# Optimization experiments

Measured on AMD Instinct MI355X. Metric: run time of the kernel, lower is better.

The kernel has to match this reference:

```python
import jax, jax.numpy as jnp
import numpy as np

EPS = 1e-5

def conv2d(x, w, b, groups=1):
    out = jax.lax.conv_general_dilated(
        x, w, (1, 1), 'SAME',
        dimension_numbers=('NCHW', 'OIHW', 'NCHW'),
        feature_group_count=groups)
    return out + b[None, :, None, None]

def bilinear_gather(img, ys, xs):
    # img [B,C,H,W]; ys,xs [B,K,H,W] float sample coords; zero padding outside
    H, W = img.shape[2], img.shape[3]
    y0 = jnp.floor(ys)
    x0 = jnp.floor(xs)
    wy = ys - y0
    wx = xs - x0

    def corner(yi, xi, w):
        valid = (yi >= 0) & (yi <= H - 1) & (xi >= 0) & (xi <= W - 1)
        yc = jnp.clip(yi, 0, H - 1).astype(jnp.int32)
        xc = jnp.clip(xi, 0, W - 1).astype(jnp.int32)
        # gather -> [B,C,K,H,W]
        v = jax.vmap(lambda im, y, x: im[:, y, x])(img, yc, xc)
        return v * (w * valid)[:, None]

    return (corner(y0, x0, (1 - wy) * (1 - wx))
            + corner(y0, x0 + 1, (1 - wy) * wx)
            + corner(y0 + 1, x0, wy * (1 - wx))
            + corner(y0 + 1, x0 + 1, wy * wx))

def deform_conv(x, offset, w, b):
    # torchvision DeformConv2d, kernel 3x3, stride 1, pad 1; offset layout [B,2*K,H,W] as (dy,dx) per tap
    B, C, H, W = x.shape
    K = 9
    ky = (jnp.repeat(jnp.arange(3), 3) - 1).astype(x.dtype)  # [9]
    kx = (jnp.tile(jnp.arange(3), 3) - 1).astype(x.dtype)
    off = offset.reshape(B, K, 2, H, W)
    base_y = jnp.arange(H, dtype=x.dtype)[None, None, :, None]
    base_x = jnp.arange(W, dtype=x.dtype)[None, None, None, :]
    ys = base_y + ky[None, :, None, None] + off[:, :, 0]  # [B,K,H,W]
    xs = base_x + kx[None, :, None, None] + off[:, :, 1]
    sampled = bilinear_gather(x, ys, xs)                  # [B,C,K,H,W]
    out = jnp.einsum('bckhw,ock->bohw', sampled, w.reshape(w.shape[0], C, K))
    return out + b[None, :, None, None]

def setup_inputs() -> dict:
    key = jax.random.key(0)
    ks = jax.random.split(key, 12)
    C, O = 128, 128
    B, H, W = 4, 96, 96
    s = 0.05
    return {
        'x': jax.random.normal(ks[0], (B, C, H, W), jnp.float32),
        'dw_w': jax.random.normal(ks[1], (C, 1, 3, 3), jnp.float32) * s,
        'dw_b': jax.random.normal(ks[2], (C,), jnp.float32) * s,
        'pw_w': jax.random.normal(ks[3], (O, C, 1, 1), jnp.float32) * s,
        'pw_b': jax.random.normal(ks[4], (O,), jnp.float32) * s,
        'off_w': jax.random.normal(ks[5], (18, O, 3, 3), jnp.float32) * s,
        'off_b': jax.random.normal(ks[6], (18,), jnp.float32) * s,
        'dc_w': jax.random.normal(ks[7], (O, O, 3, 3), jnp.float32) * s,
        'dc_b': jax.random.normal(ks[8], (O,), jnp.float32) * s,
        'ln_g': jnp.ones((O,), jnp.float32),
        'ln_b': jnp.zeros((O,), jnp.float32),
    }

def reference(x, dw_w, dw_b, pw_w, pw_b, off_w, off_b, dc_w, dc_b, ln_g, ln_b):
    C = x.shape[1]
    # depthwise-separable conv
    h = conv2d(x, dw_w, dw_b, groups=C)
    h = conv2d(h, pw_w, pw_b)
    # InstanceNorm2d (affine=False)
    mu = h.mean((2, 3), keepdims=True)
    var = h.var((2, 3), keepdims=True)
    dsc = (h - mu) * jax.lax.rsqrt(var + EPS)
    # Dropout2d: inference mode -> identity
    offset = conv2d(dsc, off_w, off_b)              # [B,18,H,W]
    dc = deform_conv(dsc, offset, dc_w, dc_b)       # [B,O,H,W]
    # LayerNorm over channels (NHWC last axis)
    nhwc = dc.transpose(0, 2, 3, 1)
    m = nhwc.mean(-1, keepdims=True)
    v = nhwc.var(-1, keepdims=True)
    ln = (nhwc - m) * jax.lax.rsqrt(v + EPS) * ln_g + ln_b
    attn = jax.nn.sigmoid(ln.transpose(0, 3, 1, 2))
    return dsc * attn
```

## Files before the change

kernel.cpp:

```cpp
#include <hip/hip_runtime.h>
#include <math.h>

#define HW 9216
#define WD 96
#define NC 128

typedef unsigned short u16;
typedef __attribute__((ext_vector_type(8))) short short8;
typedef __attribute__((ext_vector_type(4))) float v4f;

__device__ __forceinline__ int rfl(int v){ return __builtin_amdgcn_readfirstlane(v); }
__device__ __forceinline__ float bu2f(u16 s){ return __uint_as_float(((unsigned)s)<<16); }
__device__ __forceinline__ u16 f2b(float f){ unsigned u = __float_as_uint(f);
  return (u16)((u + 0x7fffu + ((u>>16)&1u))>>16); }

__global__ __launch_bounds__(256) void prep_weights(const float* __restrict__ pw_w,
    const float* __restrict__ off_w, const float* __restrict__ dc_w,
    u16* __restrict__ wpwb, u16* __restrict__ wob, u16* __restrict__ wdcb){
  int t = blockIdx.x*256 + threadIdx.x;
  if (t < 16384) wpwb[t] = f2b(pw_w[t]);
  if (t < 36864){
    int ntl = t/18432, rem = t - ntl*18432;
    int s = rem>>9, l = (rem>>3)&63, e = rem&7;
    int o = ntl*16 + (l&15);
    int c = (s&3)*32 + ((l>>4)<<3) + e;
    int k = s>>2;
    wob[t] = (o<18) ? f2b(off_w[(o*128+c)*9+k]) : (u16)0;
  }
  if (t < 147456){
    int e = t&7, l = (t>>3)&63, f = (t>>9)&7, g = t>>12;
    int s = g%18, r = g/18;
    int nt = f>>1, ks = f&1;
    int c = ((s&1)<<6) + ks*32 + ((l>>4)<<3) + e;
    int o = (r<<6) + nt*16 + (l&15);
    int k = s>>1;
    wdcb[t] = f2b(dc_w[(o*128+c)*9 + k]);
  }
}

__global__ __launch_bounds__(256) void dw_conv(const float* __restrict__ x,
    const float* __restrict__ w, const float* __restrict__ bias, u16* __restrict__ h1b){
  int n = blockIdx.x*256 + threadIdx.x;
  int bc = rfl(n / 2304);
  int qp = n - bc*2304;
  int p = qp*4;
  int c = bc & 127;
  int yy = p / WD, xx = p - yy*WD;
  const float* xc = x + (size_t)bc*HW;
  const float* wc = w + c*9;
  float bs = bias[c];
  float a0=bs, a1=bs, a2=bs, a3=bs;
  #pragma unroll
  for (int r=0;r<3;r++){
    int y2 = yy + r - 1;
    if (y2>=0 && y2<96){
      const float* row = xc + y2*WD + xx;
      float4 vc = *(const float4*)row;
      float vl = (xx>0)  ? row[-1] : 0.f;
      float vr = (xx<92) ? row[4]  : 0.f;
      float w0 = wc[r*3+0], w1 = wc[r*3+1], w2 = wc[r*3+2];
      a0 = fmaf(w0, vl,   fmaf(w1, vc.x, fmaf(w2, vc.y, a0)));
      a1 = fmaf(w0, vc.x, fmaf(w1, vc.y, fmaf(w2, vc.z, a1)));
      a2 = fmaf(w0, vc.y, fmaf(w1, vc.z, fmaf(w2, vc.w, a2)));
      a3 = fmaf(w0, vc.z, fmaf(w1, vc.w, fmaf(w2, vr,   a3)));
    }
  }
  ushort4 pk = make_ushort4(f2b(a0), f2b(a1), f2b(a2), f2b(a3));
  *(ushort4*)(h1b + (size_t)bc*HW + p) = pk;
}

__global__ __launch_bounds__(256) void pw_mfma(const u16* __restrict__ h1b,
    const u16* __restrict__ wpwb, const float* __restrict__ pw_b,
    u16* __restrict__ h2b){
  __shared__ short Aw[128*136];
  __shared__ short Bw[128*68];
  int blk = blockIdx.x; int row0 = blk*64;
  int b = rfl(row0/HW); int pbase = rfl(row0 - b*HW);
  int t = threadIdx.x;
  #pragma unroll
  for (int i=0;i<8;i++){
    int idx = i*256 + t; int o = idx>>4, seg = idx&15;
    *(short8*)&Aw[o*136 + seg*8] = *(const short8*)(wpwb + o*128 + seg*8);
  }
  #pragma unroll
  for (int i=0;i<4;i++){
    int idx = i*256 + t; int c = idx>>3, seg = idx&7;
    *(short8*)&Bw[c*68 + seg*8] =
      *(const short8*)(h1b + (size_t)(b*NC+c)*HW + pbase + seg*8);
  }
  __syncthreads();
  int w = rfl(t>>6); int l = t&63; int q = l>>4; int ln = l&15;
  v4f acc[8];
  #pragma unroll
  for (int mt=0;mt<8;mt++) acc[mt] = (v4f){0.f,0.f,0.f,0.f};
  #pragma unroll
  for (int ks=0;ks<4;ks++){
    short8 bf;
    #pragma unroll
    for (int j=0;j<8;j++) bf[j] = Bw[(ks*32 + q*8 + j)*68 + w*16 + ln];
    #pragma unroll
    for (int mt=0;mt<8;mt++){
      short8 af = *(short8*)&Aw[(mt*16+ln)*136 + ks*32 + q*8];
      acc[mt] = __builtin_amdgcn_mfma_f32_16x16x32_bf16(af, bf, acc[mt], 0,0,0);
    }
  }
  int px = pbase + w*16 + ln;
  #pragma unroll
  for (int mt=0;mt<8;mt++){
    #pragma unroll
    for (int r=0;r<4;r++){
      int o = mt*16 + q*4 + r;
      h2b[(size_t)(b*NC+o)*HW + px] = f2b(acc[mt][r] + pw_b[o]);
    }
  }
}

__global__ __launch_bounds__(256) void inorm_stats(const u16* __restrict__ h2b,
    float* __restrict__ st){
  int bc = blockIdx.x;
  const u16* src = h2b + (size_t)bc*HW;
  float s=0.f, ss=0.f;
  for (int i=threadIdx.x; i<1152; i+=256){
    short8 v8 = *(const short8*)(src + i*8);
    #pragma unroll
    for (int j=0;j<8;j++){
      float v = bu2f((u16)v8[j]);
      s += v; ss = fmaf(v,v,ss);
    }
  }
  #pragma unroll
  for (int off=32; off; off>>=1){ s += __shfl_down(s,off); ss += __shfl_down(ss,off); }
  __shared__ float rsm[2][4];
  int wave = threadIdx.x>>6, lane = threadIdx.x&63;
  if (lane==0){ rsm[0][wave]=s; rsm[1][wave]=ss; }
  __syncthreads();
  if (threadIdx.x==0){
    float S = rsm[0][0]+rsm[0][1]+rsm[0][2]+rsm[0][3];
    float SS= rsm[1][0]+rsm[1][1]+rsm[1][2]+rsm[1][3];
    float mu = S * (1.f/9216.f);
    float var = SS * (1.f/9216.f) - mu*mu;
    st[bc*2]   = mu;
    st[bc*2+1] = rsqrtf(var + 1e-5f);
  }
}

__global__ __launch_bounds__(256) void make_dsc(const u16* __restrict__ h2b,
    const float* __restrict__ st, u16* __restrict__ dscT){
  int blk = blockIdx.x;
  int pt = blk % 144; int r = blk/144; int ch = r & 1; int b = r >> 1;
  int c0 = ch*64, pbase = pt*64;
  __shared__ float tile[64][65];
  int tr = threadIdx.x >> 2;
  int g  = threadIdx.x & 3;
  int c  = c0 + tr;
  float mu = st[(b*128+c)*2];
  float rs = st[(b*128+c)*2+1];
  const u16* src = h2b + (size_t)(b*128+c)*HW + pbase + g*16;
  #pragma unroll
  for (int i=0;i<2;i++){
    short8 v8 = *(const short8*)(src + i*8);
    #pragma unroll
    for (int j=0;j<8;j++){
      float v = (bu2f((u16)v8[j]) - mu)*rs;
      tile[tr][g*16 + i*8 + j] = v;
    }
  }
  __syncthreads();
  int pr = tr;
  u16* dt = dscT + ((size_t)b*HW + pbase + pr)*NC + c0 + g*16;
  #pragma unroll
  for (int i=0;i<4;i++){
    float v0 = tile[g*16+i*4+0][pr], v1 = tile[g*16+i*4+1][pr];
    float v2 = tile[g*16+i*4+2][pr], v3 = tile[g*16+i*4+3][pr];
    ushort4 hi = make_ushort4(f2b(v0), f2b(v1), f2b(v2), f2b(v3));
    *(ushort4*)(dt + i*4) = hi;
  }
}

__global__ __launch_bounds__(256) void off_mfma(const u16* __restrict__ dscT,
    const u16* __restrict__ wobp, const float* __restrict__ off_b,
    float4* __restrict__ wg, ushort4* __restrict__ ad){
  __shared__ short As[2][32*40];
  __shared__ float Po[18*32];
  int blk = blockIdx.x;
  int tile = (blk&7)*144 + (blk>>3);
  int row0 = tile*32;
  int b = rfl(row0/HW); int pbase = rfl(row0 - b*HW);
  int t = threadIdx.x;
  bool stg = t < 128;
  int apx = (t>>2)&31, segA = t&3;
  int w = rfl(t>>6); int l = t&63; int q = l>>4; int ln = l&15;
  int mt = w&1, ntl = w>>1;
  int P = pbase + apx;
  int py = P/96, px_ = P - 96*py;
  const u16* gsrc = dscT + (size_t)b*HW*NC;
  const u16* wbase = wobp + ntl*18432 + l*8;
  uint4 rgA, rgB; short8 bregE, bregO;
  auto issue = [&](int s, uint4& rg){
    int k = s>>2, cseg = s&3;
    int y2 = py + k/3 - 1, x2 = px_ + k%3 - 1;
    bool valid = stg && ((unsigned)y2 < 96u) && ((unsigned)x2 < 96u);
    int off = ((y2*96 + x2)*NC) + cseg*32 + segA*8;
    rg = valid ? *(const uint4*)(gsrc + off) : (uint4){0,0,0,0};
  };
  auto issueB = [&](int s)->short8{
    return *(const short8*)(wbase + s*512);
  };
  auto commit = [&](int buf, uint4& rg){
    if (stg) *(short8*)&As[buf][apx*40 + segA*8] = *(short8*)&rg;
  };
  v4f acc = (v4f){0.f,0.f,0.f,0.f};
  auto step = [&](int buf, short8 bf){
    short8 ah = *(short8*)&As[buf][(mt*16+ln)*40 + q*8];
    acc = __builtin_amdgcn_mfma_f32_16x16x32_bf16(ah, bf, acc, 0,0,0);
  };
  issue(0, rgA); issue(1, rgB);
  bregE = issueB(0); bregO = issueB(1);
  commit(0, rgA);
  __syncthreads();
  #pragma unroll 1
  for (int s=0;s<36;s+=2){
    if (s+2<36) issue(s+2, rgA);
    commit(1, rgB);
    step(0, bregE);
    if (s+2<36) bregE = issueB(s+2);
    __syncthreads();
    if (s+3<36) issue(s+3, rgB);
    if (s+2<36) commit(0, rgA);
    step(1, bregO);
    if (s+3<36) bregO = issueB(s+3);
    __syncthreads();
  }
  int o = ntl*16 + ln;
  if (o < 18){
    float ob = off_b[o];
    #pragma unroll
    for (int r=0;r<4;r++) Po[o*32 + mt*16 + q*4 + r] = acc[r] + ob;
  }
  __syncthreads();
  #pragma unroll
  for (int i=0;i<2;i++){
    int idx = i*256 + t;
    if (idx < 288){
      int pxl = idx & 31, k = idx >> 5;
      int Pp = pbase + pxl;
      float dy = Po[(2*k)*32 + pxl], dx = Po[(2*k+1)*32 + pxl];
      float ys = (float)(Pp/96 + k/3 - 1) + dy;
      float xs = (float)(Pp%96 + k%3 - 1) + dx;
      float fy0 = floorf(ys), fx0 = floorf(xs);
      float wy = ys - fy0, wx = xs - fx0;
      int y0 = (int)fy0, x0 = (int)fx0;
      int y1 = y0+1, x1 = x0+1;
      float vy0 = (y0>=0 && y0<=95) ? 1.f : 0.f;
      float vy1 = (y1>=0 && y1<=95) ? 1.f : 0.f;
      float vx0 = (x0>=0 && x0<=95) ? 1.f : 0.f;
      float vx1 = (x1>=0 && x1<=95) ? 1.f : 0.f;
      int y0c=min(max(y0,0),95), y1c=min(max(y1,0),95);
      int x0c=min(max(x0,0),95), x1c=min(max(x1,0),95);
      float4 w4;
      w4.x = (1.f-wy)*(1.f-wx)*vy0*vx0;
      w4.y = (1.f-wy)*wx*vy0*vx1;
      w4.z = wy*(1.f-wx)*vy1*vx0;
      w4.w = wy*wx*vy1*vx1;
      int gi = (b*9 + k)*HW + pbase + pxl;
      wg[gi] = w4;
      ad[gi] = make_ushort4((u16)(y0c*WD+x0c), (u16)(y0c*WD+x1c),
                            (u16)(y1c*WD+x0c), (u16)(y1c*WD+x1c));
    }
  }
}

__global__ __launch_bounds__(256) void deform_mfma(const u16* __restrict__ dscT,
    const u16* __restrict__ wdcb, const float* __restrict__ dc_b,
    const float4* __restrict__ wg, const ushort4* __restrict__ ad,
    const float* __restrict__ ln_g, const float* __restrict__ ln_b,
    float* __restrict__ out){
  __shared__ short As[2][32*68];
  __shared__ float4 WgL[288];
  __shared__ ushort4 AdL[288];
  __shared__ float RS[2][4][4][4];
  __shared__ u16 DT[32*128];
  int blk = blockIdx.x;
  int tile = (blk&7)*144 + (blk>>3);
  int row0 = tile*32;
  int b = rfl(row0/HW); int pbase = rfl(row0 - b*HW);
  int t = threadIdx.x;
  int apx = t>>3, cs8 = t&7;
  int w = rfl(t>>6); int l = t&63; int q = l>>4; int ln = l&15;
  int mt = w&1, nb = (w>>1)*4, rrole = rfl(w>>1);
  const u16* db0 = dscT + (size_t)b*HW*NC + cs8*8;
  const u16* wbase = wdcb + (size_t)rrole*(18*4096) + l*8;
  #pragma unroll
  for (int i=0;i<2;i++){
    int idx = i*256 + t;
    if (idx < 288){ int k = idx>>5, pxl = idx&31; int gi = (b*9+k)*HW + pbase + pxl;
      WgL[idx] = wg[gi]; AdL[idx] = ad[gi]; }
  }
  __syncthreads();
  uint4 gA0,gA1,gA2,gA3, gB0,gB1,gB2,gB3;
  float4 wvA, wvB;
  short8 bregE[8], bregO[8];
  auto issueG = [&](int s, float4& wv, uint4& r0, uint4& r1, uint4& r2, uint4& r3){
    int k = s>>1, cb = (s&1)<<6;
    ushort4 av = AdL[k*32+apx]; wv = WgL[k*32+apx];
    const u16* db = db0 + cb;
    r0 = *(const uint4*)(db + (int)av.x*NC);
    r1 = *(const uint4*)(db + (int)av.y*NC);
    r2 = *(const uint4*)(db + (int)av.z*NC);
    r3 = *(const uint4*)(db + (int)av.w*NC);
  };
  auto issueB = [&](int s, short8* dst){
    const u16* p = wbase + s*4096;
    #pragma unroll
    for (int f=0;f<8;f++) dst[f] = *(const short8*)(p + f*512);
  };
  auto commitA = [&](int buf, float4 wv, uint4& r0, uint4& r1, uint4& r2, uint4& r3){
    const u16* pa=(const u16*)&r0; const u16* pb=(const u16*)&r1;
    const u16* pc=(const u16*)&r2; const u16* pd=(const u16*)&r3;
    short8 sv;
    #pragma unroll
    for (int j=0;j<8;j++){
      float f = wv.x*bu2f(pa[j]) + wv.y*bu2f(pb[j]) + wv.z*bu2f(pc[j]) + wv.w*bu2f(pd[j]);
      sv[j] = (short)f2b(f);
    }
    *(short8*)&As[buf][apx*68 + cs8*8] = sv;
  };
  v4f acc[4];
  #pragma unroll
  for (int nt=0;nt<4;nt++) acc[nt] = (v4f){0.f,0.f,0.f,0.f};
  auto step = [&](int buf, const short8* bb){
    #pragma unroll
    for (int ks=0;ks<2;ks++){
      short8 af = *(const short8*)&As[buf][(mt*16+ln)*68 + ks*32 + q*8];
      #pragma unroll
      for (int nt=0;nt<4;nt++)
        acc[nt] = __builtin_amdgcn_mfma_f32_16x16x32_bf16(af, bb[nt*2+ks], acc[nt], 0,0,0);
    }
  };
  issueG(0, wvA, gA0,gA1,gA2,gA3); issueB(0, bregE);
  issueG(1, wvB, gB0,gB1,gB2,gB3); issueB(1, bregO);
  commitA(0, wvA, gA0,gA1,gA2,gA3);
  __syncthreads();
  #pragma unroll 1
  for (int s=0;s<18;s+=2){
    if (s+2<18) issueG(s+2, wvA, gA0,gA1,gA2,gA3);
    commitA(1, wvB, gB0,gB1,gB2,gB3);
    step(0, bregE);
    if (s+2<18) issueB(s+2, bregE);
    __syncthreads();
    if (s+3<18) issueG(s+3, wvB, gB0,gB1,gB2,gB3);
    if (s+2<18) commitA(0, wvA, gA0,gA1,gA2,gA3);
    step(1, bregO);
    if (s+3<18) issueB(s+3, bregO);
    __syncthreads();
  }
  int o_[4]; float bias_[4], g_[4], bb_[4];
  #pragma unroll
  for (int nt=0;nt<4;nt++){
    int o = (nb+nt)*16 + ln;
    o_[nt] = o; bias_[nt] = dc_b[o]; g_[nt] = ln_g[o]; bb_[nt] = ln_b[o];
  }
  float s_[4] = {0.f,0.f,0.f,0.f}, ss_[4] = {0.f,0.f,0.f,0.f};
  #pragma unroll
  for (int r=0;r<4;r++){
    #pragma unroll
    for (int nt=0;nt<4;nt++){
      float v = acc[nt][r] + bias_[nt];
      s_[r] += v; ss_[r] = fmaf(v, v, ss_[r]);
    }
  }
  #pragma unroll
  for (int off=1; off<16; off<<=1){
    #pragma unroll
    for (int r=0;r<4;r++){
      s_[r]  += __shfl_xor(s_[r],  off);
      ss_[r] += __shfl_xor(ss_[r], off);
    }
  }
  if (ln==0){
    #pragma unroll
    for (int r=0;r<4;r++){ RS[0][w][q][r] = s_[r]; RS[1][w][q][r] = ss_[r]; }
  }
  {
    const u16* dsrc = dscT + ((size_t)b*HW + pbase)*NC;
    #pragma unroll
    for (int i=0;i<2;i++){
      int idx = i*256 + t;
      *(short8*)&DT[idx*8] = *(const short8*)(dsrc + idx*8);
    }
  }
  __syncthreads();
  float m_[4], rs_[4];
  #pragma unroll
  for (int r=0;r<4;r++){
    float S  = RS[0][w][q][r] + RS[0][w^2][q][r];
    float SS = RS[1][w][q][r] + RS[1][w^2][q][r];
    float m = S*(1.f/128.f);
    float var = SS*(1.f/128.f) - m*m;
    m_[r] = m; rs_[r] = rsqrtf(var + 1e-5f);
  }
  int pxb = pbase + mt*16 + q*4;
  int lpx = mt*16 + q*4;
  #pragma unroll
  for (int nt=0;nt<4;nt++){
    size_t base = (size_t)(b*NC + o_[nt])*HW + pxb;
    float4 ov;
    #pragma unroll
    for (int r=0;r<4;r++){
      float v = acc[nt][r] + bias_[nt];
      float lnv = (v - m_[r])*rs_[r]*g_[nt] + bb_[nt];
      float attn = 1.f/(1.f+__expf(-lnv));
      float dv = bu2f(DT[(lpx+r)*128 + o_[nt]]);
      ((float*)&ov)[r] = dv * attn;
    }
    *(float4*)(out + base) = ov;
  }
}

extern "C" void kernel_launch(void* const* d_in, const int* in_sizes, int n_in,
                              void* d_out, int out_size, void* d_ws, size_t ws_size,
                              hipStream_t stream){
  const float* x    = (const float*)d_in[0];
  const float* dw_w = (const float*)d_in[1];
  const float* dw_b = (const float*)d_in[2];
  const float* pw_w = (const float*)d_in[3];
  const float* pw_b = (const float*)d_in[4];
  const float* off_w= (const float*)d_in[5];
  const float* off_b= (const float*)d_in[6];
  const float* dc_w = (const float*)d_in[7];
  const float* dc_b = (const float*)d_in[8];
  const float* ln_g = (const float*)d_in[9];
  const float* ln_b = (const float*)d_in[10];
  float* out = (float*)d_out;

  float* W    = (float*)d_ws;
  u16*     h1b  = (u16*)W;
  u16*     h2b  = (u16*)(W + 4718592);
  u16*     dscT = (u16*)(W + 9437184);
  float4*  wg   = (float4*)(W + 14155776);
  ushort4* ad   = (ushort4*)(W + 15482880);
  float*   st   = W + 16146432;
  u16*     wpwb = (u16*)(W + 16147456);
  u16*     wob  = (u16*)(W + 16155648);
  u16*     wdcb = (u16*)(W + 16174080);

  prep_weights<<<576, 256, 0, stream>>>(pw_w, off_w, dc_w, wpwb, wob, wdcb);
  dw_conv     <<<4608, 256, 0, stream>>>(x, dw_w, dw_b, h1b);
  pw_mfma     <<<576, 256, 0, stream>>>(h1b, wpwb, pw_b, h2b);
  inorm_stats <<<512, 256, 0, stream>>>(h2b, st);
  make_dsc    <<<1152, 256, 0, stream>>>(h2b, st, dscT);
  off_mfma    <<<1152, 256, 0, stream>>>(dscT, wob, off_b, wg, ad);
  deform_mfma <<<1152, 256, 0, stream>>>(dscT, wdcb, dc_b, wg, ad, ln_g, ln_b, out);
}
```

Baseline: 171.8 us.

## Stage full 128-channel tap per step in offset conv MFMA pipeline

The offset-conv kernel now stages all 128 channels of one 3x3 tap per pipeline step instead of 32 channels. All 256 threads take part in staging rather than half, and each step issues four MFMAs. This cuts the loop from 36 to 9 steps and removes most of the barriers. In exchange it uses more LDS (row stride 136) and holds more weight registers per thread, which may lower occupancy.

```diff
diff --git a/kernel.cpp b/kernel.cpp
--- a/kernel.cpp
+++ b/kernel.cpp
@@ -180,56 +180,65 @@
 __global__ __launch_bounds__(256) void off_mfma(const u16* __restrict__ dscT,
     const u16* __restrict__ wobp, const float* __restrict__ off_b,
     float4* __restrict__ wg, ushort4* __restrict__ ad){
-  __shared__ short As[2][32*40];
+  __shared__ short As[2][32*136];
   __shared__ float Po[18*32];
   int blk = blockIdx.x;
   int tile = (blk&7)*144 + (blk>>3);
   int row0 = tile*32;
   int b = rfl(row0/HW); int pbase = rfl(row0 - b*HW);
   int t = threadIdx.x;
-  bool stg = t < 128;
-  int apx = (t>>2)&31, segA = t&3;
+  int apx = t>>3, seg8 = t&7;
   int w = rfl(t>>6); int l = t&63; int q = l>>4; int ln = l&15;
   int mt = w&1, ntl = w>>1;
   int P = pbase + apx;
   int py = P/96, px_ = P - 96*py;
   const u16* gsrc = dscT + (size_t)b*HW*NC;
   const u16* wbase = wobp + ntl*18432 + l*8;
-  uint4 rgA, rgB; short8 bregE, bregO;
-  auto issue = [&](int s, uint4& rg){
-    int k = s>>2, cseg = s&3;
+  uint4 rgA0, rgA1, rgB0, rgB1;
+  short8 bregE[4], bregO[4];
+  const uint4 Z = (uint4){0,0,0,0};
+  auto issueG = [&](int k, uint4& r0, uint4& r1){
     int y2 = py + k/3 - 1, x2 = px_ + k%3 - 1;
-    bool valid = stg && ((unsigned)y2 < 96u) && ((unsigned)x2 < 96u);
-    int off = ((y2*96 + x2)*NC) + cseg*32 + segA*8;
-    rg = valid ? *(const uint4*)(gsrc + off) : (uint4){0,0,0,0};
-  };
-  auto issueB = [&](int s)->short8{
-    return *(const short8*)(wbase + s*512);
-  };
-  auto commit = [&](int buf, uint4& rg){
-    if (stg) *(short8*)&As[buf][apx*40 + segA*8] = *(short8*)&rg;
+    bool valid = ((unsigned)y2 < 96u) && ((unsigned)x2 < 96u);
+    int off = (y2*96 + x2)*NC + seg8*8;
+    r0 = valid ? *(const uint4*)(gsrc + off) : Z;
+    r1 = valid ? *(const uint4*)(gsrc + off + 64) : Z;
+  };
+  auto issueB = [&](int k, short8* dst){
+    #pragma unroll
+    for (int cs=0; cs<4; cs++) dst[cs] = *(const short8*)(wbase + (k*4+cs)*512);
+  };
+  auto commit = [&](int buf, uint4& r0, uint4& r1){
+    *(short8*)&As[buf][apx*136 + seg8*8] = *(short8*)&r0;
+    *(short8*)&As[buf][apx*136 + 64 + seg8*8] = *(short8*)&r1;
   };
   v4f acc = (v4f){0.f,0.f,0.f,0.f};
-  auto step = [&](int buf, short8 bf){
-    short8 ah = *(short8*)&As[buf][(mt*16+ln)*40 + q*8];
-    acc = __builtin_amdgcn_mfma_f32_16x16x32_bf16(ah, bf, acc, 0,0,0);
-  };
-  issue(0, rgA); issue(1, rgB);
-  bregE = issueB(0); bregO = issueB(1);
-  commit(0, rgA);
+  auto step = [&](int buf, const short8* bb){
+    #pragma unroll
+    for (int cs=0; cs<4; cs++){
+      short8 af = *(const short8*)&As[buf][(mt*16+ln)*136 + cs*32 + q*8];
+      acc = __builtin_amdgcn_mfma_f32_16x16x32_bf16(af, bb[cs], acc, 0,0,0);
+    }
+  };
+  issueG(0, rgA0, rgA1); issueB(0, bregE);
+  issueG(1, rgB0, rgB1); issueB(1, bregO);
+  commit(0, rgA0, rgA1);
   __syncthreads();
   #pragma unroll 1
-  for (int s=0;s<36;s+=2){
-    if (s+2<36) issue(s+2, rgA);
-    commit(1, rgB);
+  for (int k=0;k<9;k+=2){
+    bool m1 = (k+1<9), m2 = (k+2<9), m3 = (k+3<9);
+    if (m2) issueG(k+2, rgA0, rgA1);
+    if (m1) commit(1, rgB0, rgB1);
     step(0, bregE);
-    if (s+2<36) bregE = issueB(s+2);
+    if (m2) issueB(k+2, bregE);
     __syncthreads();
-    if (s+3<36) issue(s+3, rgB);
-    if (s+2<36) commit(0, rgA);
-    step(1, bregO);
-    if (s+3<36) bregO = issueB(s+3);
-    __syncthreads();
+    if (m1){
+      if (m3) issueG(k+3, rgB0, rgB1);
+      if (m2) commit(0, rgA0, rgA1);
+      step(1, bregO);
+      if (m3) issueB(k+3, bregO);
+      __syncthreads();
+    }
   }
   int o = ntl*16 + ln;
   if (o < 18){
```

Result: no change. 169.2 us (-1.5%).
